# Kernel tuning notes

Measured on AMD Instinct MI355X. Metric: run time of the kernel, lower is better.

## Reference

```python
import jax, jax.numpy as jnp
from jax import lax
import numpy as np

K = 32        # self.k: neighbors queried per center
TOP = 5       # inner topk size (hardcoded in source)
MAX_ITER = 16 # bound on the data-dependent while loop; leftovers emitted at final iter


def _refine_one(pc, centers, ids):
    """Vectorized translation of the per-batch while-loop.

    Instead of shrinking the sample set each iteration (data-dependent shape),
    every sample is tracked with an `active` flag and a convergence-iteration
    stamp. Emitting order in the torch code is (iteration, surviving-order),
    and boolean masking preserves relative original order, so a stable sort by
    (conv_iter, original_index) reproduces the exact concatenation order.
    """
    N, D = pc.shape
    S = centers.shape[0]
    ar = jnp.arange(S)

    def knn(q):  # q: [S,3] -> [S,K] indices of nearest cloud points (ascending dist)
        d2 = jnp.sum((q[:, None, :] - pc[None, :, :]) ** 2, axis=-1)  # [S,N]
        _, ind = lax.top_k(-d2, K)
        return ind

    def step(cur_pts, cur_idx):
        ind = knn(cur_pts)                                   # [S,K]
        nbh = pc[ind]                                        # [S,K,3]
        gc = jnp.mean(nbh, axis=1)                           # [S,3]
        dist = jnp.linalg.norm(nbh - gc[:, None, :], axis=2) # [S,K]
        _, top = lax.top_k(-dist, TOP)                       # [S,TOP] smallest dists
        in_top = jnp.any(top == 0, axis=1)                   # center (col 0) stable?
        new_idx = ind[ar, top[:, 0]]                         # point closest to centroid
        return ind, in_top, new_idx

    def body(it, st):
        cur_pts, cur_idx, conv_it, out_pts, out_idx, out_grp, active = st
        ind, in_top, new_idx = step(cur_pts, cur_idx)
        newly = active & in_top
        conv_it = jnp.where(newly, it, conv_it)
        out_pts = jnp.where(newly[:, None], cur_pts, out_pts)
        out_idx = jnp.where(newly, cur_idx, out_idx)
        out_grp = jnp.where(newly[:, None], ind, out_grp)
        move = active & ~in_top
        cur_idx = jnp.where(move, new_idx, cur_idx)
        cur_pts = jnp.where(move[:, None], pc[new_idx], cur_pts)
        return (cur_pts, cur_idx, conv_it, out_pts, out_idx, out_grp, move)

    st0 = (centers, ids,
           jnp.full((S,), MAX_ITER, jnp.int32),
           jnp.zeros((S, D), pc.dtype),
           jnp.zeros((S,), ids.dtype),
           jnp.zeros((S, K), jnp.int32),
           jnp.ones((S,), bool))
    cur_pts, cur_idx, conv_it, out_pts, out_idx, out_grp, active = lax.fori_loop(
        0, MAX_ITER, body, st0)

    # force-emit any sample that never converged within MAX_ITER
    ind, _, _ = step(cur_pts, cur_idx)
    out_pts = jnp.where(active[:, None], cur_pts, out_pts)
    out_idx = jnp.where(active, cur_idx, out_idx)
    out_grp = jnp.where(active[:, None], ind, out_grp)

    order = jnp.argsort(conv_it * (S + 1) + ar)  # stable (iter, orig-pos) order
    return out_pts[order], out_idx[order], out_grp[order]


def setup_inputs() -> dict:
    key = jax.random.key(0)
    k1, k2, k3 = jax.random.split(key, 3)
    B, N, S = 8, 8192, 1024
    xyz = jax.random.normal(k1, (B, N, 3), jnp.float32)
    center = jax.random.normal(k2, (B, S, 3), jnp.float32)
    idx = jax.random.randint(k3, (B, S), 0, N, jnp.int32)
    return {"xyz": xyz, "center": center, "idx": idx}


def reference(xyz, center, idx):
    assert xyz.shape[0] == center.shape[0]
    C, I1, I2 = jax.vmap(_refine_one)(xyz, center, idx)
    # torch runs under no_grad; outputs are detached constants
    return (lax.stop_gradient(C), I1, I2)
```

## Files before the change

### kernel.cpp

```cpp
#include <hip/hip_runtime.h>
#include <stdint.h>

#define BATCH   8
#define NPTS    8192
#define SCH     1024
#define KNN     32
#define TOPC    5
#define MAXIT   16
#define NCELL   4096
#define NGRP    128
#define NSEED   6

typedef unsigned long long ull;
typedef float vf2 __attribute__((ext_vector_type(2)));
typedef float vf4 __attribute__((ext_vector_type(4)));

#define SENTKEY ((((ull)0x7F800000u) << 13) | 0x1FFFull)

__device__ __forceinline__ uint32_t xshfl32(uint32_t v, int xl) {
    if (xl == 1)
        return (uint32_t)__builtin_amdgcn_update_dpp((int)v, (int)v, 0xB1, 0xF, 0xF, true);
    if (xl == 2)
        return (uint32_t)__builtin_amdgcn_update_dpp((int)v, (int)v, 0x4E, 0xF, 0xF, true);
    return (uint32_t)__shfl_xor((int)v, xl, 64);
}
__device__ __forceinline__ ull xshfl64(ull v, int xl) {
    uint32_t lo = xshfl32((uint32_t)v, xl);
    uint32_t hi = xshfl32((uint32_t)(v >> 32), xl);
    return ((ull)hi << 32) | lo;
}
__device__ __forceinline__ float xshflf(float v, int xl) {
    return __uint_as_float(xshfl32(__float_as_uint(v), xl));
}

__device__ __forceinline__ float d2_exact(vf4 q, vf4 p) {
#pragma clang fp contract(off)
    vf2 d = q.xy - p.xy;
    vf2 s = d * d;
    float dz = q.z - p.z;
    float sz = dz * dz;
    return (s.x + s.y) + sz;
}

__device__ __forceinline__ void insert_top4(ull key, ull& k0, ull& k1, ull& k2,
                                            ull& k3, float& th) {
    if (key < k3) {
        k3 = key;
        { bool c = k3 < k2; ull mn = c ? k3 : k2, mx = c ? k2 : k3; k2 = mn; k3 = mx; }
        { bool c = k2 < k1; ull mn = c ? k2 : k1, mx = c ? k1 : k2; k1 = mn; k2 = mx; }
        { bool c = k1 < k0; ull mn = c ? k1 : k0, mx = c ? k0 : k1; k0 = mn; k1 = mx; }
        th = __uint_as_float((uint32_t)(k3 >> 13));
    }
}

__device__ __forceinline__ ull wave_min_u64(ull k) {
#pragma unroll
    for (int off = 32; off; off >>= 1) {
        ull o = xshfl64(k, off);
        k = o < k ? o : k;
    }
    return k;
}
__device__ __forceinline__ ull wave_max_u64(ull k) {
#pragma unroll
    for (int off = 32; off; off >>= 1) {
        ull o = xshfl64(k, off);
        k = o > k ? o : k;
    }
    return k;
}

__device__ __forceinline__ float bbox_mind2(vf4 q, vf4 c, vf4 h) {
    float dx = fmaxf(fabsf(q.x - c.x) - h.x, 0.f);
    float dy = fmaxf(fabsf(q.y - c.y) - h.y, 0.f);
    float dz = fmaxf(fabsf(q.z - c.z) - h.z, 0.f);
    return (dx * dx + dy * dy + dz * dz) * 0.9999f;
}

__device__ __forceinline__ ull cx(ull v, int xl, bool keepmin) {
    ull o = xshfl64(v, xl);
    return ((v < o) == keepmin) ? v : o;
}
__device__ __forceinline__ void cswap(ull& a, ull& b, bool up) {
    bool lt = a < b;
    ull mn = lt ? a : b, mx = lt ? b : a;
    a = up ? mn : mx;
    b = up ? mx : mn;
}

__device__ __forceinline__ uint32_t cx32(uint32_t v, int xl, bool keepmin) {
    uint32_t o = xshfl32(v, xl);
    return ((v < o) == keepmin) ? v : o;
}
__device__ __forceinline__ void cswap32(uint32_t& a, uint32_t& b, bool up) {
    uint32_t mn = a < b ? a : b, mx = a < b ? b : a;
    a = up ? mn : mx;
    b = up ? mx : mn;
}

__device__ __forceinline__ void sort128_u32(uint32_t& s0, uint32_t& s1, int lane) {
    cswap32(s0, s1, true);
    if (lane & 1) { uint32_t t = s0; s0 = s1; s1 = t; }
#pragma unroll
    for (int kk = 4; kk <= 128; kk <<= 1) {
        const bool up = (lane & (kk >> 1)) == 0;
#pragma unroll
        for (int d = kk >> 1; d >= 2; d >>= 1) {
            const int xl = d >> 1;
            const bool keepmin = (up == ((lane & xl) == 0));
            s0 = cx32(s0, xl, keepmin);
            s1 = cx32(s1, xl, keepmin);
        }
        cswap32(s0, s1, up);
    }
}

__device__ __forceinline__ int next_gid(ull& r0, ull& r1) {
    if (r0) { int g = __ffsll((unsigned long long)r0) - 1; r0 &= r0 - 1; return g; }
    if (r1) { int g = __ffsll((unsigned long long)r1) - 1; r1 &= r1 - 1; return 64 + g; }
    return -1;
}

__device__ __forceinline__ int cell_of(float x, float y, float z) {
    int cxi = min(15, max(0, (int)floorf((x + 4.0f) * 2.0f)));
    int cyi = min(15, max(0, (int)floorf((y + 4.0f) * 2.0f)));
    int czi = min(15, max(0, (int)floorf((z + 4.0f) * 2.0f)));
    uint32_t sx = (cxi & 1) | ((cxi & 2) << 2) | ((cxi & 4) << 4) | ((cxi & 8) << 6);
    uint32_t sy = (cyi & 1) | ((cyi & 2) << 2) | ((cyi & 4) << 4) | ((cyi & 8) << 6);
    uint32_t sz = (czi & 1) | ((czi & 2) << 2) | ((czi & 4) << 4) | ((czi & 8) << 6);
    return (int)(sx | (sy << 1) | (sz << 2));
}

__device__ __attribute__((noinline)) int serial_topk_masked(
    const vf4* __restrict__ Psort, vf4 q, int lane, ull sm0, ull sm1) {
    ull k0 = SENTKEY, k1 = SENTKEY, k2 = SENTKEY, k3 = SENTKEY;
    int s0 = 0, s1 = 0, s2 = 0, s3 = 0;
    float th = __builtin_inff();
    for (int gid = 0; gid < NGRP; ++gid) {
        bool sel = (gid < 64) ? ((sm0 >> gid) & 1ull) : ((sm1 >> (gid - 64)) & 1ull);
        if (!sel) continue;
        vf4 p = Psort[(gid << 6) + lane];
        float d2 = d2_exact(q, p);
        uint32_t oi = __float_as_uint(p.w);
        ull key = ((ull)__float_as_uint(d2) << 13) | oi;
        if (d2 <= th && key < k3) {
            k3 = key; s3 = gid;
            if (k3 < k2) { ull t = k2; k2 = k3; k3 = t; int ts = s2; s2 = s3; s3 = ts; }
            if (k2 < k1) { ull t = k1; k1 = k2; k2 = t; int ts = s1; s1 = s2; s2 = ts; }
            if (k1 < k0) { ull t = k0; k0 = k1; k1 = t; int ts = s0; s0 = s1; s1 = ts; }
            th = __uint_as_float((uint32_t)(k3 >> 13));
        }
    }
    ull em0 = 0ull, em1 = 0ull;
    int cnt = 4, my_ind = 0;
    for (int r = 0; r < KNN; ++r) {
        ull gmin = wave_min_u64(k0);
        int widx = (int)(gmin & 0x1FFFull);
        if (lane == r) my_ind = widx;
        if (k0 == gmin) {
            int g = s0;
            if (g < 64) em0 |= 1ull << g; else em1 |= 1ull << (g - 64);
            k0 = k1; k1 = k2; k2 = k3; k3 = SENTKEY;
            s0 = s1; s1 = s2; s2 = s3;
            if (--cnt == 0) {
                k0 = k1 = k2 = k3 = SENTKEY;
                float th2 = __builtin_inff();
                for (int gid = 0; gid < NGRP; ++gid) {
                    bool sel = (gid < 64) ? ((sm0 >> gid) & 1ull)
                                          : ((sm1 >> (gid - 64)) & 1ull);
                    bool ex = (gid < 64) ? ((em0 >> gid) & 1ull)
                                         : ((em1 >> (gid - 64)) & 1ull);
                    if (!sel || ex) continue;
                    vf4 p = Psort[(gid << 6) + lane];
                    float d2 = d2_exact(q, p);
                    uint32_t oi = __float_as_uint(p.w);
                    ull key = ((ull)__float_as_uint(d2) << 13) | oi;
                    if (d2 <= th2 && key < k3) {
                        k3 = key; s3 = gid;
                        if (k3 < k2) { ull t = k2; k2 = k3; k3 = t; int ts = s2; s2 = s3; s3 = ts; }
                        if (k2 < k1) { ull t = k1; k1 = k2; k2 = t; int ts = s1; s1 = s2; s2 = ts; }
                        if (k1 < k0) { ull t = k0; k0 = k1; k1 = t; int ts = s0; s0 = s1; s1 = ts; }
                        th2 = __uint_as_float((uint32_t)(k3 >> 13));
                    }
                }
                cnt = 4;
            }
        }
    }
    return my_ind;
}

__global__ __launch_bounds__(256) void prep_kernel(const float* __restrict__ xyz,
                                                   vf4* __restrict__ pc4,
                                                   int* __restrict__ counts) {
    int i = (int)(blockIdx.x * blockDim.x + threadIdx.x);
    if (i >= BATCH * NPTS) return;
    vf4 v;
    v.x = xyz[(size_t)i * 3 + 0];
    v.y = xyz[(size_t)i * 3 + 1];
    v.z = xyz[(size_t)i * 3 + 2];
    v.w = 0.f;
    pc4[i] = v;
    int b = i >> 13;
    atomicAdd(&counts[b * NCELL + cell_of(v.x, v.y, v.z)], 1);
}

__global__ __launch_bounds__(1024) void scan_kernel(const int* __restrict__ counts,
                                                    int* __restrict__ cursor) {
    int b = (int)blockIdx.x, tid = (int)threadIdx.x;
    __shared__ int part[1024];
    int base = b * NCELL + tid * 4;
    int v0 = counts[base], v1 = counts[base + 1], v2 = counts[base + 2], v3 = counts[base + 3];
    int s = v0 + v1 + v2 + v3;
    part[tid] = s;
    __syncthreads();
    for (int off = 1; off < 1024; off <<= 1) {
        int t = (tid >= off) ? part[tid - off] : 0;
        __syncthreads();
        part[tid] += t;
        __syncthreads();
    }
    int excl = part[tid] - s;
    cursor[base] = excl;
    cursor[base + 1] = excl + v0;
    cursor[base + 2] = excl + v0 + v1;
    cursor[base + 3] = excl + v0 + v1 + v2;
}

__global__ __launch_bounds__(256) void scatter_kernel(const vf4* __restrict__ pc4,
                                                      int* __restrict__ cursor,
                                                      vf4* __restrict__ sortedP) {
    int i = (int)(blockIdx.x * blockDim.x + threadIdx.x);
    if (i >= BATCH * NPTS) return;
    vf4 v = pc4[i];
    int b = i >> 13, pi = i & (NPTS - 1);
    int c = cell_of(v.x, v.y, v.z);
    int pos = atomicAdd(&cursor[b * NCELL + c], 1);
    v.w = __uint_as_float((uint32_t)pi);
    sortedP[((size_t)b << 13) + pos] = v;
}

__global__ __launch_bounds__(256) void bbox_kernel(const vf4* __restrict__ sortedP,
                                                   vf4* __restrict__ bC,
                                                   vf4* __restrict__ bH) {
    int g = (int)((blockIdx.x * blockDim.x + threadIdx.x) >> 6);
    int lane = (int)(threadIdx.x & 63);
    vf4 p = sortedP[((size_t)g << 6) + lane];
    float mnx = p.x, mxx = p.x, mny = p.y, mxy = p.y, mnz = p.z, mxz = p.z;
#pragma unroll
    for (int off = 32; off; off >>= 1) {
        mnx = fminf(mnx, xshflf(mnx, off));
        mxx = fmaxf(mxx, xshflf(mxx, off));
        mny = fminf(mny, xshflf(mny, off));
        mxy = fmaxf(mxy, xshflf(mxy, off));
        mnz = fminf(mnz, xshflf(mnz, off));
        mxz = fmaxf(mxz, xshflf(mxz, off));
    }
    if (lane == 0) {
        vf4 c, h;
        c.x = (mnx + mxx) * 0.5f; c.y = (mny + mxy) * 0.5f; c.z = (mnz + mxz) * 0.5f; c.w = 0.f;
        h.x = (mxx - mnx) * 0.5f; h.y = (mxy - mny) * 0.5f; h.z = (mxz - mnz) * 0.5f; h.w = 0.f;
        bC[g] = c;
        bH[g] = h;
    }
}

__global__ __launch_bounds__(256)
__attribute__((amdgpu_waves_per_eu(2, 4)))
void refine_kernel(
    const vf4* __restrict__ pc4, const vf4* __restrict__ sortedP,
    const vf4* __restrict__ bC, const vf4* __restrict__ bH,
    const float* __restrict__ center, const int* __restrict__ idx_in,
    float* __restrict__ pts_ws, int* __restrict__ idx_ws,
    int* __restrict__ grp_ws, int* __restrict__ conv_ws) {
    const int lane = (int)(threadIdx.x & 63);
    const int w = (int)(threadIdx.x >> 6);
    const int b = (int)(blockIdx.x & 7);
    const int s = (((int)blockIdx.x >> 3) << 2) + w;
    const vf4* __restrict__ Porig = pc4 + ((size_t)b << 13);
    const vf4* __restrict__ Psort = sortedP + ((size_t)b << 13);

    __shared__ vf4 sbC[NGRP], sbH[NGRP];
    __shared__ vf4 nbh[4][KNN];

    {
        const int t = (int)threadIdx.x;
        if (t < NGRP) sbC[t] = bC[(b << 7) + t];
        else          sbH[t - NGRP] = bH[(b << 7) + (t - NGRP)];
    }
    __syncthreads();

    const size_t ch = ((size_t)b << 10) + (size_t)s;
    vf4 q;
    q.x = center[ch * 3 + 0];
    q.y = center[ch * 3 + 1];
    q.z = center[ch * 3 + 2];
    q.w = 0.f;
    int qidx = idx_in[ch];

    int conv = MAXIT;
    int my_ind = 0;
    vf4 myp = q;
    bool warm = false;

    for (int it = 0;; ++it) {
        const vf4 c0 = sbC[lane],      h0 = sbH[lane];
        const vf4 c1 = sbC[64 + lane], h1 = sbH[64 + lane];
        const float m0 = bbox_mind2(q, c0, h0);
        const float m1 = bbox_mind2(q, c1, h1);

        ull k0 = SENTKEY, k1 = SENTKEY, k2 = SENTKEY, k3 = SENTKEY;
        float th = __builtin_inff();
        ull sm0 = 0ull, sm1 = 0ull, am0 = 0ull, am1 = 0ull;
        float th0 = __builtin_inff();

        bool fastwarm = false;
        if (warm) {
            const float dw = (lane < KNN) ? d2_exact(q, myp) : 0.f;
            th0 = dw;
#pragma unroll
            for (int off = 32; off; off >>= 1)
                th0 = fmaxf(th0, xshflf(th0, off));
            sm0 = __ballot(m0 <= th0);
            sm1 = __ballot(m1 <= th0);
            const int nsel = __popcll(sm0) + __popcll(sm1);
            if (nsel <= 20) { fastwarm = true; am0 = sm0; am1 = sm1; }
        }

        if (!fastwarm) {
            sm0 = 0ull; sm1 = 0ull;
            uint32_t g0k = ((__float_as_uint(m0) >> 6) << 7) | (uint32_t)lane;
            uint32_t g1k = ((__float_as_uint(m1) >> 6) << 7) | (uint32_t)(64 + lane);
            sort128_u32(g0k, g1k, lane);
#pragma unroll
            for (int r = 0; r < NSEED; ++r) {
                const uint32_t nk = (r & 1)
                    ? (uint32_t)__shfl((int)g1k, r >> 1, 64)
                    : (uint32_t)__shfl((int)g0k, r >> 1, 64);
                const int gid = (int)(nk & 127u);
                if (gid < 64) sm0 |= 1ull << gid; else sm1 |= 1ull << (gid - 64);
                const vf4 p = Psort[(gid << 6) + lane];
                const float d2 = d2_exact(q, p);
                if (d2 <= th)
                    insert_top4(((ull)__float_as_uint(d2) << 13) | __float_as_uint(p.w),
                                k0, k1, k2, k3, th);
            }
            ull t = k0;
            {
                ull o = xshfl64(t, 32);
                t = o < t ? o : t;
            }
            const ull B = wave_max_u64(t);
            const float Bd = fminf(__uint_as_float((uint32_t)(B >> 13)), th0);
            am0 = __ballot(m0 <= Bd) & ~sm0;
            am1 = __ballot(m1 <= Bd) & ~sm1;
            sm0 |= am0; sm1 |= am1;
        }

        {
            ull rem0 = am0, rem1 = am1;
            int ga = next_gid(rem0, rem1);
            while (ga >= 0) {
                const int gb = next_gid(rem0, rem1);
                const vf4 pa = Psort[(ga << 6) + lane];
                vf4 pb;
                if (gb >= 0) pb = Psort[(gb << 6) + lane];
                const float da = d2_exact(q, pa);
                if (da <= th)
                    insert_top4(((ull)__float_as_uint(da) << 13) | __float_as_uint(pa.w),
                                k0, k1, k2, k3, th);
                if (gb >= 0) {
                    const float dbv = d2_exact(q, pb);
                    if (dbv <= th)
                        insert_top4(((ull)__float_as_uint(dbv) << 13) | __float_as_uint(pb.w),
                                    k0, k1, k2, k3, th);
                }
                ga = next_gid(rem0, rem1);
            }
        }
        const ull prek3 = k3;

        const bool odd = (lane & 1) != 0;
        ull a0 = odd ? k3 : k0;
        ull a1 = odd ? k2 : k1;
        ull a2 = odd ? k1 : k2;
        ull a3 = odd ? k0 : k3;
#pragma unroll
        for (int kk = 8; kk <= 256; kk <<= 1) {
            const bool up = (lane & (kk >> 2)) == 0;
#pragma unroll
            for (int d = kk >> 1; d >= 4; d >>= 1) {
                const int xl = d >> 2;
                const bool keepmin = (up == ((lane & xl) == 0));
                a0 = cx(a0, xl, keepmin);
                a1 = cx(a1, xl, keepmin);
                a2 = cx(a2, xl, keepmin);
                a3 = cx(a3, xl, keepmin);
            }
            cswap(a0, a2, up); cswap(a1, a3, up);
            cswap(a0, a1, up); cswap(a2, a3, up);
        }
        const ull tau = (ull)__shfl((unsigned long long)a3, 7, 64);
        const ull bad = __ballot(prek3 < tau);
        if (bad != 0ull) {
            my_ind = serial_topk_masked(Psort, q, lane, sm0, sm1);
        } else {
            const int src = lane >> 2;
            const uint32_t lo0 = (uint32_t)__shfl((int)(uint32_t)a0, src, 64);
            const uint32_t lo1 = (uint32_t)__shfl((int)(uint32_t)a1, src, 64);
            const uint32_t lo2 = (uint32_t)__shfl((int)(uint32_t)a2, src, 64);
            const uint32_t lo3 = (uint32_t)__shfl((int)(uint32_t)a3, src, 64);
            const int sel = lane & 3;
            uint32_t lo = (sel == 0) ? lo0 : (sel == 1) ? lo1 : (sel == 2) ? lo2 : lo3;
            my_ind = (int)(lo & 0x1FFFu);
        }

        if (it == MAXIT) break;

        myp = q;
        if (lane < KNN) {
            myp = Porig[my_ind];
            nbh[w][lane] = myp;
        }
        __asm__ volatile("s_waitcnt lgkmcnt(0)" ::: "memory");
        float sx = 0.f, sy = 0.f, sz = 0.f;
#pragma unroll
        for (int j = 0; j < KNN; ++j) {
            vf4 pj = nbh[w][j];
            sx = __fadd_rn(sx, pj.x);
            sy = __fadd_rn(sy, pj.y);
            sz = __fadd_rn(sz, pj.z);
        }
        const float gx = __fmul_rn(sx, 0.03125f);
        const float gy = __fmul_rn(sy, 0.03125f);
        const float gz = __fmul_rn(sz, 0.03125f);

        float dj = __builtin_inff();
        if (lane < KNN) {
            const float dx = __fsub_rn(myp.x, gx);
            const float dy = __fsub_rn(myp.y, gy);
            const float dz = __fsub_rn(myp.z, gz);
            dj = sqrtf(__fadd_rn(__fadd_rn(__fmul_rn(dx, dx), __fmul_rn(dy, dy)),
                                 __fmul_rn(dz, dz)));
        }
        const uint32_t db = __float_as_uint(dj);
        const uint32_t d0 = (uint32_t)__shfl((int)db, 0, 64);
        const ull bal = __ballot(db < d0);
        if (__popcll(bal) <= TOPC - 1) { conv = it; break; }

        uint32_t m = db;
#pragma unroll
        for (int off = 32; off; off >>= 1) {
            uint32_t o = xshfl32(m, off);
            m = o < m ? o : m;
        }
        const ull balm = __ballot(db == m);
        const int jm = __ffsll((unsigned long long)balm) - 1;
        qidx = __shfl(my_ind, jm, 64);
        q.x = __shfl(myp.x, jm, 64);
        q.y = __shfl(myp.y, jm, 64);
        q.z = __shfl(myp.z, jm, 64);
        q.w = 0.f;
        warm = true;
    }

    if (lane < KNN) grp_ws[ch * KNN + lane] = my_ind;
    if (lane == 0) {
        pts_ws[ch * 3 + 0] = q.x;
        pts_ws[ch * 3 + 1] = q.y;
        pts_ws[ch * 3 + 2] = q.z;
        idx_ws[ch] = qidx;
        conv_ws[ch] = conv;
    }
}

__global__ __launch_bounds__(1024) void order_kernel(
    const float* __restrict__ pts_ws, const int* __restrict__ idx_ws,
    const int* __restrict__ grp_ws, const int* __restrict__ conv_ws,
    float* __restrict__ out) {
    const int b = (int)blockIdx.x;
    const int s = (int)threadIdx.x;
    const int w = s >> 6, l = s & 63;
    __shared__ int wavecnt[16][MAXIT + 1];
    __shared__ int binbase[MAXIT + 1];
    const size_t ch = (size_t)b * SCH + s;
    const int c = conv_ws[ch];
    int rw = 0;
#pragma unroll
    for (int v = 0; v <= MAXIT; ++v) {
        ull bal = __ballot(c == v);
        if (l == 0) wavecnt[w][v] = (int)__popcll(bal);
        if (c == v) rw = (int)__popcll(bal & ((1ull << l) - 1ull));
    }
    __syncthreads();
    if (s == 0) {
        int acc = 0;
        for (int v = 0; v <= MAXIT; ++v) {
            int t = 0;
            for (int w2 = 0; w2 < 16; ++w2) t += wavecnt[w2][v];
            binbase[v] = acc;
            acc += t;
        }
    }
    __syncthreads();
    int pos = binbase[c] + rw;
    for (int w2 = 0; w2 < w; ++w2) pos += wavecnt[w2][c];

    float* __restrict__ C  = out;
    float* __restrict__ I1 = out + (size_t)BATCH * SCH * 3;
    float* __restrict__ I2 = I1 + (size_t)BATCH * SCH;
    const size_t o = (size_t)b * SCH + pos;
    C[o * 3 + 0] = pts_ws[ch * 3 + 0];
    C[o * 3 + 1] = pts_ws[ch * 3 + 1];
    C[o * 3 + 2] = pts_ws[ch * 3 + 2];
    I1[o] = (float)idx_ws[ch];
#pragma unroll
    for (int k = 0; k < KNN; ++k) I2[o * KNN + k] = (float)grp_ws[ch * KNN + k];
}

extern "C" void kernel_launch(void* const* d_in, const int* in_sizes, int n_in,
                              void* d_out, int out_size, void* d_ws, size_t ws_size,
                              hipStream_t stream) {
    const float* xyz    = (const float*)d_in[0];
    const float* center = (const float*)d_in[1];
    const int*   idx_in = (const int*)d_in[2];
    float* out = (float*)d_out;

    char* wp = (char*)d_ws;
    vf4* pc4     = (vf4*)wp;  wp += (size_t)BATCH * NPTS * sizeof(vf4);
    vf4* sortedP = (vf4*)wp;  wp += (size_t)BATCH * NPTS * sizeof(vf4);
    vf4* bC      = (vf4*)wp;  wp += (size_t)BATCH * NGRP * sizeof(vf4);
    vf4* bH      = (vf4*)wp;  wp += (size_t)BATCH * NGRP * sizeof(vf4);
    int* counts  = (int*)wp;  wp += (size_t)BATCH * NCELL * 4;
    int* cursor  = (int*)wp;  wp += (size_t)BATCH * NCELL * 4;
    float* pts_ws = (float*)wp; wp += (size_t)BATCH * SCH * 3 * 4;
    int*   idx_ws = (int*)wp;   wp += (size_t)BATCH * SCH * 4;
    int*   grp_ws = (int*)wp;   wp += (size_t)BATCH * SCH * KNN * 4;
    int*   conv_ws = (int*)wp;

    hipMemsetAsync(counts, 0, (size_t)BATCH * NCELL * 4, stream);
    prep_kernel<<<(BATCH * NPTS + 255) / 256, 256, 0, stream>>>(xyz, pc4, counts);
    scan_kernel<<<BATCH, 1024, 0, stream>>>(counts, cursor);
    scatter_kernel<<<(BATCH * NPTS + 255) / 256, 256, 0, stream>>>(pc4, cursor, sortedP);
    bbox_kernel<<<(BATCH * NGRP * 64) / 256, 256, 0, stream>>>(sortedP, bC, bH);

    const int chains = BATCH * SCH;
    refine_kernel<<<chains * 64 / 256, 256, 0, stream>>>(
        pc4, sortedP, bC, bH, center, idx_in, pts_ws, idx_ws, grp_ws, conv_ws);
    order_kernel<<<BATCH, SCH, 0, stream>>>(pts_ws, idx_ws, grp_ws, conv_ws, out);
}
```

Measured before the change: 191.4 us.

## Fuse scan/scatter/bbox kernels, add parallel fallback top-k and rotated group loads

Merges the scan, scatter and bounding-box kernels into one per-batch kernel using a wave-shuffle scan and LDS cursors, cutting two launches and the global cursor traffic. Replaces the serial masked top-k fallback with a parallel collect-then-bitonic-sort path that gathers candidates under the threshold into a shared buffer, keeping the serial path only on overflow. Rotates the lane-to-point mapping per group in the refine loads, apparently to vary access patterns. The fused build runs only 8 blocks, which risks serialising work that was previously spread wide.

```diff
diff --git a/kernel.cpp b/kernel.cpp
--- a/kernel.cpp
+++ b/kernel.cpp
@@ -10,12 +10,15 @@
 #define NCELL   4096
 #define NGRP    128
 #define NSEED   6
+#define FCAP    128
 
 typedef unsigned long long ull;
 typedef float vf2 __attribute__((ext_vector_type(2)));
 typedef float vf4 __attribute__((ext_vector_type(4)));
 
 #define SENTKEY ((((ull)0x7F800000u) << 13) | 0x1FFFull)
+
+#define ROTL(lane, g) (((lane) + (g) * 17) & 63)
 
 __device__ __forceinline__ uint32_t xshfl32(uint32_t v, int xl) {
     if (xl == 1)
@@ -112,6 +115,23 @@
             s1 = cx32(s1, xl, keepmin);
         }
         cswap32(s0, s1, up);
+    }
+}
+
+__device__ __forceinline__ void sort128_u64(ull& s0, ull& s1, int lane) {
+    cswap(s0, s1, true);
+    if (lane & 1) { ull t = s0; s0 = s1; s1 = t; }
+#pragma unroll
+    for (int kk = 4; kk <= 128; kk <<= 1) {
+        const bool up = (lane & (kk >> 1)) == 0;
+#pragma unroll
+        for (int d = kk >> 1; d >= 2; d >>= 1) {
+            const int xl = d >> 1;
+            const bool keepmin = (up == ((lane & xl) == 0));
+            s0 = cx(s0, xl, keepmin);
+            s1 = cx(s1, xl, keepmin);
+        }
+        cswap(s0, s1, up);
     }
 }
 
@@ -190,6 +210,35 @@
     return my_ind;
 }
 
+__device__ int collect_topk(const vf4* __restrict__ Psort, vf4 q, int lane,
+                            ull sm0, ull sm1, ull tau,
+                            ull* buf, int* cnt) {
+    if (lane == 0) *cnt = 0;
+    __asm__ volatile("s_waitcnt lgkmcnt(0)" ::: "memory");
+    ull r0 = sm0, r1 = sm1;
+    int g = next_gid(r0, r1);
+    while (g >= 0) {
+        vf4 p = Psort[(g << 6) + lane];
+        float d2 = d2_exact(q, p);
+        ull key = ((ull)__float_as_uint(d2) << 13) | __float_as_uint(p.w);
+        if (key <= tau) {
+            int pos = atomicAdd(cnt, 1);
+            if (pos < FCAP) buf[pos] = key;
+        }
+        g = next_gid(r0, r1);
+    }
+    __asm__ volatile("s_waitcnt lgkmcnt(0)" ::: "memory");
+    const int M = *cnt;
+    if (M > FCAP) return -1;
+    ull s0 = (2 * lane + 0 < M) ? buf[2 * lane + 0] : SENTKEY;
+    ull s1 = (2 * lane + 1 < M) ? buf[2 * lane + 1] : SENTKEY;
+    sort128_u64(s0, s1, lane);
+    const int src = lane >> 1;
+    const uint32_t e0 = (uint32_t)__shfl((int)(uint32_t)s0, src, 64);
+    const uint32_t e1 = (uint32_t)__shfl((int)(uint32_t)s1, src, 64);
+    return (int)(((lane & 1) ? e1 : e0) & 0x1FFFu);
+}
+
 __global__ __launch_bounds__(256) void prep_kernel(const float* __restrict__ xyz,
                                                    vf4* __restrict__ pc4,
                                                    int* __restrict__ counts) {
@@ -205,63 +254,69 @@
     atomicAdd(&counts[b * NCELL + cell_of(v.x, v.y, v.z)], 1);
 }
 
-__global__ __launch_bounds__(1024) void scan_kernel(const int* __restrict__ counts,
-                                                    int* __restrict__ cursor) {
-    int b = (int)blockIdx.x, tid = (int)threadIdx.x;
-    __shared__ int part[1024];
-    int base = b * NCELL + tid * 4;
-    int v0 = counts[base], v1 = counts[base + 1], v2 = counts[base + 2], v3 = counts[base + 3];
-    int s = v0 + v1 + v2 + v3;
-    part[tid] = s;
+__global__ __launch_bounds__(1024) void sortbuild_kernel(
+    const vf4* __restrict__ pc4, const int* __restrict__ counts,
+    vf4* __restrict__ sortedP, vf4* __restrict__ bC, vf4* __restrict__ bH) {
+    const int b = (int)blockIdx.x;
+    const int t = (int)threadIdx.x, lane = t & 63, w = t >> 6;
+    __shared__ int cur[NCELL];
+    __shared__ int wsum[16];
+
+    const int base = t * 4;
+    const int gb = b * NCELL + base;
+    const int v0 = counts[gb], v1 = counts[gb + 1], v2 = counts[gb + 2], v3 = counts[gb + 3];
+    const int s = v0 + v1 + v2 + v3;
+    int incl = s;
+#pragma unroll
+    for (int off = 1; off < 64; off <<= 1) {
+        int o = __shfl_up(incl, off, 64);
+        if (lane >= off) incl += o;
+    }
+    if (lane == 63) wsum[w] = incl;
     __syncthreads();
-    for (int off = 1; off < 1024; off <<= 1) {
-        int t = (tid >= off) ? part[tid - off] : 0;
-        __syncthreads();
-        part[tid] += t;
-        __syncthreads();
-    }
-    int excl = part[tid] - s;
-    cursor[base] = excl;
-    cursor[base + 1] = excl + v0;
-    cursor[base + 2] = excl + v0 + v1;
-    cursor[base + 3] = excl + v0 + v1 + v2;
-}
-
-__global__ __launch_bounds__(256) void scatter_kernel(const vf4* __restrict__ pc4,
-                                                      int* __restrict__ cursor,
-                                                      vf4* __restrict__ sortedP) {
-    int i = (int)(blockIdx.x * blockDim.x + threadIdx.x);
-    if (i >= BATCH * NPTS) return;
-    vf4 v = pc4[i];
-    int b = i >> 13, pi = i & (NPTS - 1);
-    int c = cell_of(v.x, v.y, v.z);
-    int pos = atomicAdd(&cursor[b * NCELL + c], 1);
-    v.w = __uint_as_float((uint32_t)pi);
-    sortedP[((size_t)b << 13) + pos] = v;
-}
-
-__global__ __launch_bounds__(256) void bbox_kernel(const vf4* __restrict__ sortedP,
-                                                   vf4* __restrict__ bC,
-                                                   vf4* __restrict__ bH) {
-    int g = (int)((blockIdx.x * blockDim.x + threadIdx.x) >> 6);
-    int lane = (int)(threadIdx.x & 63);
-    vf4 p = sortedP[((size_t)g << 6) + lane];
-    float mnx = p.x, mxx = p.x, mny = p.y, mxy = p.y, mnz = p.z, mxz = p.z;
-#pragma unroll
-    for (int off = 32; off; off >>= 1) {
-        mnx = fminf(mnx, xshflf(mnx, off));
-        mxx = fmaxf(mxx, xshflf(mxx, off));
-        mny = fminf(mny, xshflf(mny, off));
-        mxy = fmaxf(mxy, xshflf(mxy, off));
-        mnz = fminf(mnz, xshflf(mnz, off));
-        mxz = fmaxf(mxz, xshflf(mxz, off));
-    }
-    if (lane == 0) {
-        vf4 c, h;
-        c.x = (mnx + mxx) * 0.5f; c.y = (mny + mxy) * 0.5f; c.z = (mnz + mxz) * 0.5f; c.w = 0.f;
-        h.x = (mxx - mnx) * 0.5f; h.y = (mxy - mny) * 0.5f; h.z = (mxz - mnz) * 0.5f; h.w = 0.f;
-        bC[g] = c;
-        bH[g] = h;
+    if (t == 0) {
+        int acc = 0;
+#pragma unroll
+        for (int i = 0; i < 16; ++i) { int x = wsum[i]; wsum[i] = acc; acc += x; }
+    }
+    __syncthreads();
+    const int excl = incl - s + wsum[w];
+    cur[base]     = excl;
+    cur[base + 1] = excl + v0;
+    cur[base + 2] = excl + v0 + v1;
+    cur[base + 3] = excl + v0 + v1 + v2;
+    __syncthreads();
+
+#pragma unroll
+    for (int k = 0; k < 8; ++k) {
+        const int i = k * 1024 + t;
+        vf4 v = pc4[((size_t)b << 13) + i];
+        const int c = cell_of(v.x, v.y, v.z);
+        const int pos = atomicAdd(&cur[c], 1);
+        v.w = __uint_as_float((uint32_t)i);
+        sortedP[((size_t)b << 13) + pos] = v;
+    }
+    __syncthreads();
+
+    for (int g = w; g < NGRP; g += 16) {
+        vf4 p = sortedP[((size_t)b << 13) + (g << 6) + lane];
+        float mnx = p.x, mxx = p.x, mny = p.y, mxy = p.y, mnz = p.z, mxz = p.z;
+#pragma unroll
+        for (int off = 32; off; off >>= 1) {
+            mnx = fminf(mnx, xshflf(mnx, off));
+            mxx = fmaxf(mxx, xshflf(mxx, off));
+            mny = fminf(mny, xshflf(mny, off));
+            mxy = fmaxf(mxy, xshflf(mxy, off));
+            mnz = fminf(mnz, xshflf(mnz, off));
+            mxz = fmaxf(mxz, xshflf(mxz, off));
+        }
+        if (lane == 0) {
+            vf4 c, h;
+            c.x = (mnx + mxx) * 0.5f; c.y = (mny + mxy) * 0.5f; c.z = (mnz + mxz) * 0.5f; c.w = 0.f;
+            h.x = (mxx - mnx) * 0.5f; h.y = (mxy - mny) * 0.5f; h.z = (mxz - mnz) * 0.5f; h.w = 0.f;
+            bC[(b << 7) + g] = c;
+            bH[(b << 7) + g] = h;
+        }
     }
 }
 
@@ -282,6 +337,8 @@
 
     __shared__ vf4 sbC[NGRP], sbH[NGRP];
     __shared__ vf4 nbh[4][KNN];
+    __shared__ ull fbuf[4][FCAP];
+    __shared__ int fcnt[4];
 
     {
         const int t = (int)threadIdx.x;
@@ -339,7 +396,7 @@
                     : (uint32_t)__shfl((int)g0k, r >> 1, 64);
                 const int gid = (int)(nk & 127u);
                 if (gid < 64) sm0 |= 1ull << gid; else sm1 |= 1ull << (gid - 64);
-                const vf4 p = Psort[(gid << 6) + lane];
+                const vf4 p = Psort[(gid << 6) + ROTL(lane, gid)];
                 const float d2 = d2_exact(q, p);
                 if (d2 <= th)
                     insert_top4(((ull)__float_as_uint(d2) << 13) | __float_as_uint(p.w),
@@ -361,15 +418,15 @@
             ull rem0 = am0, rem1 = am1;
             int ga = next_gid(rem0, rem1);
             while (ga >= 0) {
-                const int gb = next_gid(rem0, rem1);
-                const vf4 pa = Psort[(ga << 6) + lane];
+                const int gb2 = next_gid(rem0, rem1);
+                const vf4 pa = Psort[(ga << 6) + ROTL(lane, ga)];
                 vf4 pb;
-                if (gb >= 0) pb = Psort[(gb << 6) + lane];
+                if (gb2 >= 0) pb = Psort[(gb2 << 6) + ROTL(lane, gb2)];
                 const float da = d2_exact(q, pa);
                 if (da <= th)
                     insert_top4(((ull)__float_as_uint(da) << 13) | __float_as_uint(pa.w),
                                 k0, k1, k2, k3, th);
-                if (gb >= 0) {
+                if (gb2 >= 0) {
                     const float dbv = d2_exact(q, pb);
                     if (dbv <= th)
                         insert_top4(((ull)__float_as_uint(dbv) << 13) | __float_as_uint(pb.w),
@@ -403,7 +460,9 @@
         const ull tau = (ull)__shfl((unsigned long long)a3, 7, 64);
         const ull bad = __ballot(prek3 < tau);
         if (bad != 0ull) {
-            my_ind = serial_topk_masked(Psort, q, lane, sm0, sm1);
+            const int mi = collect_topk(Psort, q, lane, sm0, sm1, tau,
+                                        fbuf[w], &fcnt[w]);
+            my_ind = (mi >= 0) ? mi : serial_topk_masked(Psort, q, lane, sm0, sm1);
         } else {
             const int src = lane >> 2;
             const uint32_t lo0 = (uint32_t)__shfl((int)(uint32_t)a0, src, 64);
@@ -532,7 +591,6 @@
     vf4* bC      = (vf4*)wp;  wp += (size_t)BATCH * NGRP * sizeof(vf4);
     vf4* bH      = (vf4*)wp;  wp += (size_t)BATCH * NGRP * sizeof(vf4);
     int* counts  = (int*)wp;  wp += (size_t)BATCH * NCELL * 4;
-    int* cursor  = (int*)wp;  wp += (size_t)BATCH * NCELL * 4;
     float* pts_ws = (float*)wp; wp += (size_t)BATCH * SCH * 3 * 4;
     int*   idx_ws = (int*)wp;   wp += (size_t)BATCH * SCH * 4;
     int*   grp_ws = (int*)wp;   wp += (size_t)BATCH * SCH * KNN * 4;
@@ -540,9 +598,7 @@
 
     hipMemsetAsync(counts, 0, (size_t)BATCH * NCELL * 4, stream);
     prep_kernel<<<(BATCH * NPTS + 255) / 256, 256, 0, stream>>>(xyz, pc4, counts);
-    scan_kernel<<<BATCH, 1024, 0, stream>>>(counts, cursor);
-    scatter_kernel<<<(BATCH * NPTS + 255) / 256, 256, 0, stream>>>(pc4, cursor, sortedP);
-    bbox_kernel<<<(BATCH * NGRP * 64) / 256, 256, 0, stream>>>(sortedP, bC, bH);
+    sortbuild_kernel<<<BATCH, 1024, 0, stream>>>(pc4, counts, sortedP, bC, bH);
 
     const int chains = BATCH * SCH;
     refine_kernel<<<chains * 64 / 256, 256, 0, stream>>>(
```

After: 188.6 us. Within noise of the previous version (-1.5%).
